# Performance work log

Hardware: AMD Instinct MI355X
Metric: run time of the kernel (lower is better)

The kernel has to match this reference:

```python
import jax, jax.numpy as jnp
import numpy as np
import math

B, N0 = 128, 128          # graphs, nodes per graph
EPG = 512                 # edges per graph
F_IN, EDGE_DIM = 64, 16
EMB, HEADS = 128, 4
HC = EMB * HEADS
L = 2                     # stacked layers (pooling every layer: top_k_every_n=1)
RATIO = 0.5
DENSE = 256


def setup_inputs():
    rng = np.random.default_rng(0)

    def U(fan_in, *shape):
        s = 1.0 / np.sqrt(fan_in)
        return jnp.asarray(rng.uniform(-s, s, shape), dtype=jnp.float32)

    x = jnp.asarray(rng.standard_normal((B * N0, F_IN)), dtype=jnp.float32)
    src = rng.integers(0, N0, (B, EPG))
    dst = rng.integers(0, N0, (B, EPG))
    off = (np.arange(B) * N0)[:, None]
    edge_index = jnp.asarray(np.stack([(src + off).reshape(-1), (dst + off).reshape(-1)]), dtype=jnp.int32)
    edge_attr = jnp.asarray(rng.standard_normal((B * EPG, EDGE_DIM)), dtype=jnp.float32)

    inp = dict(x=x, edge_index=edge_index, edge_attr=edge_attr)
    inp.update(
        c1_Wq=U(F_IN, F_IN, HC), c1_bq=U(F_IN, HC),
        c1_Wk=U(F_IN, F_IN, HC), c1_bk=U(F_IN, HC),
        c1_Wv=U(F_IN, F_IN, HC), c1_bv=U(F_IN, HC),
        c1_We=U(EDGE_DIM, EDGE_DIM, HC),
        c1_Ws=U(F_IN, F_IN, HC), c1_bs=U(F_IN, HC),
        c1_Wb=U(3 * HC, 3 * HC),
        t1_W=U(HC, HC, EMB), t1_b=U(HC, EMB),
        bn1_g=jnp.ones(EMB), bn1_b=jnp.zeros(EMB),
        cl_Wq=U(EMB, L, EMB, HC), cl_bq=U(EMB, L, HC),
        cl_Wk=U(EMB, L, EMB, HC), cl_bk=U(EMB, L, HC),
        cl_Wv=U(EMB, L, EMB, HC), cl_bv=U(EMB, L, HC),
        cl_We=U(EDGE_DIM, L, EDGE_DIM, HC),
        cl_Ws=U(EMB, L, EMB, HC), cl_bs=U(EMB, L, HC),
        cl_Wb=U(3 * HC, L, 3 * HC),
        tl_W=U(HC, L, HC, EMB), tl_b=U(HC, L, EMB),
        bnl_g=jnp.ones((L, EMB)), bnl_b=jnp.zeros((L, EMB)),
        pool_w=U(EMB, L, EMB),
        l1_W=U(2 * EMB, 2 * EMB, DENSE), l1_b=U(2 * EMB, DENSE),
        l2_W=U(DENSE, DENSE, DENSE // 2), l2_b=U(DENSE, DENSE // 2),
        l3_W=U(DENSE // 2, DENSE // 2, 1), l3_b=U(DENSE // 2, 1),
    )
    return inp


def _tconv(x, src, dst, emask, ea, Wq, bq, Wk, bk, Wv, bv, We, Ws, bs, Wb, n_nodes):
    # PyG TransformerConv, beta=True, concat=True, edge features added to key and value
    H, C = HEADS, EMB
    q = (x @ Wq + bq).reshape(-1, H, C)
    k = (x @ Wk + bk).reshape(-1, H, C)
    v = (x @ Wv + bv).reshape(-1, H, C)
    e = (ea @ We).reshape(-1, H, C)
    kj = k[src] + e
    alpha = (q[dst] * kj).sum(-1) * (1.0 / math.sqrt(C))  # [E, H]
    mx = jax.ops.segment_max(jnp.where(emask[:, None], alpha, -jnp.inf), dst, num_segments=n_nodes)
    mx = jnp.where(jnp.isfinite(mx), mx, 0.0)
    p = jnp.where(emask[:, None], jnp.exp(alpha - mx[dst]), 0.0)
    p = p / (jax.ops.segment_sum(p, dst, num_segments=n_nodes)[dst] + 1e-16)
    msg = v[src] + e
    out = jax.ops.segment_sum(p[:, :, None] * msg, dst, num_segments=n_nodes).reshape(-1, H * C)
    skip = x @ Ws + bs
    beta = jax.nn.sigmoid(jnp.concatenate([out, skip, out - skip], -1) @ Wb)[:, None]
    return beta * skip + (1.0 - beta) * out


def _bn(x, g, b):
    # BatchNorm1d, training-mode batch statistics (biased variance)
    m = x.mean(0)
    v = ((x - m) ** 2).mean(0)
    return g * (x - m) * jax.lax.rsqrt(v + 1e-5) + b


def _topk_pool(x, src, dst, emask, w, n):
    # TopKPooling: score = x.w/|w|, keep top ceil(ratio*n) per graph, scale by tanh(score)
    k = int(math.ceil(RATIO * n))
    s = (x @ w) / jnp.linalg.norm(w)          # [B*n]
    _, idx = jax.lax.top_k(s.reshape(B, n), k)
    idx = jnp.sort(idx, axis=1)
    gidx = (jnp.arange(B)[:, None] * n + idx).reshape(-1)
    x_new = x[gidx] * jnp.tanh(s[gidx])[:, None]
    kept = jnp.zeros(B * n, bool).at[gidx].set(True)
    new_id = (jnp.cumsum(kept) - 1).astype(jnp.int32)
    em = emask & kept[src] & kept[dst]
    src_n = jnp.where(em, new_id[src], 0)
    dst_n = jnp.where(em, new_id[dst], 0)
    return x_new, src_n, dst_n, em, k


def _forward(edge_index, x, edge_attr, c1_Wq, c1_bq, c1_Wk, c1_bk, c1_Wv, c1_bv, c1_We, c1_Ws, c1_bs, c1_Wb,
             t1_W, t1_b, bn1_g, bn1_b, cl_Wq, cl_bq, cl_Wk, cl_bk, cl_Wv, cl_bv, cl_We, cl_Ws, cl_bs, cl_Wb,
             tl_W, tl_b, bnl_g, bnl_b, pool_w, l1_W, l1_b, l2_W, l2_b, l3_W, l3_b):
    src, dst = edge_index[0], edge_index[1]
    emask = jnp.ones(src.shape[0], bool)
    n = N0
    x = _tconv(x, src, dst, emask, edge_attr, c1_Wq, c1_bq, c1_Wk, c1_bk, c1_Wv, c1_bv, c1_We, c1_Ws, c1_bs, c1_Wb, B * n)
    x = _bn(jax.nn.relu(x @ t1_W + t1_b), bn1_g, bn1_b)
    reps = []
    for i in range(L):
        x = _tconv(x, src, dst, emask, edge_attr, cl_Wq[i], cl_bq[i], cl_Wk[i], cl_bk[i], cl_Wv[i], cl_bv[i],
                   cl_We[i], cl_Ws[i], cl_bs[i], cl_Wb[i], B * n)
        x = _bn(jax.nn.relu(x @ tl_W[i] + tl_b[i]), bnl_g[i], bnl_b[i])
        x, src, dst, emask, n = _topk_pool(x, src, dst, emask, pool_w[i], n)
        xg = x.reshape(B, n, EMB)
        reps.append(jnp.concatenate([xg.max(1), xg.mean(1)], -1))  # gmp || gap
    h = reps[0]
    for r in reps[1:]:
        h = h + r
    h = jax.nn.relu(h @ l1_W + l1_b)  # dropout p=0.8 is identity at eval
    h = jax.nn.relu(h @ l2_W + l2_b)
    return h @ l3_W + l3_b            # [B, 1]


def reference(x, edge_index, edge_attr, c1_Wq, c1_bq, c1_Wk, c1_bk, c1_Wv, c1_bv, c1_We, c1_Ws, c1_bs, c1_Wb,
              t1_W, t1_b, bn1_g, bn1_b, cl_Wq, cl_bq, cl_Wk, cl_bk, cl_Wv, cl_bv, cl_We, cl_Ws, cl_bs, cl_Wb,
              tl_W, tl_b, bnl_g, bnl_b, pool_w, l1_W, l1_b, l2_W, l2_b, l3_W, l3_b):
    return _forward(edge_index, x, edge_attr, c1_Wq, c1_bq, c1_Wk, c1_bk, c1_Wv, c1_bv, c1_We, c1_Ws, c1_bs, c1_Wb,
                    t1_W, t1_b, bn1_g, bn1_b, cl_Wq, cl_bq, cl_Wk, cl_bk, cl_Wv, cl_bv, cl_We, cl_Ws, cl_bs, cl_Wb,
                    tl_W, tl_b, bnl_g, bnl_b, pool_w, l1_W, l1_b, l2_W, l2_b, l3_W, l3_b)
```

## Files before the change

kernel.cpp:

```cpp
#include <hip/hip_runtime.h>
#include <math.h>

#define E_TOT 65536
#define B_G   128
#define QLD   1664
#define NCOL  1792

typedef __attribute__((ext_vector_type(8))) short short8;
typedef __attribute__((ext_vector_type(4))) short short4v;
typedef __attribute__((ext_vector_type(4))) float float4v;

__device__ __forceinline__ unsigned short f2bf(float f) {
    unsigned int u = __float_as_uint(f);
    unsigned int r = u + 0x7FFFu + ((u >> 16) & 1u);
    return (unsigned short)(r >> 16);
}
__device__ __forceinline__ float bf2f(unsigned short h) {
    return __uint_as_float(((unsigned int)h) << 16);
}

struct LayerPrep {
    const float *Ws, *bs_, *Wq, *bq, *We, *Wv, *bv, *tW;
    float *Wst, *ws_z, *sbt, *zb, *Wu, *bu, *Wet, *wez, *Wvt, *bvt, *Wvz, *bvz, *tWT;
    unsigned short *Whi, *Wlo;
    int Fin;
};

__device__ __forceinline__ LayerPrep pick(const LayerPrep& p0, const LayerPrep& p1,
                                          const LayerPrep& p2) {
    return blockIdx.y == 0 ? p0 : (blockIdx.y == 1 ? p1 : p2);
}

__global__ void twt_all_k(LayerPrep p0, LayerPrep p1, LayerPrep p2) {
    LayerPrep p = pick(p0, p1, p2);
    int idx = blockIdx.x * 256 + threadIdx.x;
    int m = idx & 127, c = idx >> 7;
    p.tWT[m * 512 + c] = p.tW[idx];
}

__global__ void prep_all_k(LayerPrep p0, LayerPrep p1, LayerPrep p2, const float* Wb0,
                           const float* Wb1, const float* Wb2) {
    LayerPrep p = pick(p0, p1, p2);
    const float* Wb = blockIdx.y == 0 ? Wb0 : (blockIdx.y == 1 ? Wb1 : Wb2);
    int Fin = p.Fin;
    int w = (blockIdx.x * blockDim.x + threadIdx.x) >> 6;
    int lane = threadIdx.x & 63;
    int o1 = Fin * 128, o2 = o1 + Fin, o3 = o2 + 128, o4 = o3 + 1;
    int o5 = o4 + Fin * 64, o6 = o5 + 64, o7 = o6 + 8192, o8 = o7 + 64;
    int o9 = o8 + Fin * 512, o10 = o9 + 512, o11 = o10 + Fin * 4, total = o11 + 4;
    if (w >= total) return;
    const float *Ws = p.Ws, *bs = p.bs_, *tWT = p.tWT, *Wq = p.Wq, *bq = p.bq,
                *We = p.We, *Wv = p.Wv, *bv = p.bv;
    float s = 0.f;
    if (w < o1) {
        int f = w >> 7, m = w & 127;
        for (int c = lane; c < 512; c += 64)
            s = fmaf(Ws[(size_t)f * 512 + c], tWT[(size_t)m * 512 + c], s);
    } else if (w < o2) {
        int f = w - o1;
        for (int c = lane; c < 512; c += 64)
            s = fmaf(Ws[(size_t)f * 512 + c], Wb[512 + c] - Wb[1024 + c], s);
    } else if (w < o3) {
        int m = w - o2;
        for (int c = lane; c < 512; c += 64)
            s = fmaf(bs[c], tWT[(size_t)m * 512 + c], s);
    } else if (w < o4) {
        for (int c = lane; c < 512; c += 64)
            s = fmaf(bs[c], Wb[512 + c] - Wb[1024 + c], s);
    } else if (w < o5) {
        int q = w - o4; int f = q >> 6; int j2 = q & 63;
        int j = j2 & 15; int cb = (j2 >> 4) * 128;
        s = Wq[(size_t)f * 512 + cb + lane] * We[j * 512 + cb + lane]
          + Wq[(size_t)f * 512 + cb + lane + 64] * We[j * 512 + cb + lane + 64];
    } else if (w < o6) {
        int j2 = w - o5; int j = j2 & 15; int cb = (j2 >> 4) * 128;
        s = bq[cb + lane] * We[j * 512 + cb + lane]
          + bq[cb + lane + 64] * We[j * 512 + cb + lane + 64];
    } else if (w < o7) {
        int q = w - o6; int j2 = q >> 7; int m = q & 127;
        int j = j2 & 15; int cb = (j2 >> 4) * 128;
        s = We[j * 512 + cb + lane] * tWT[(size_t)m * 512 + cb + lane]
          + We[j * 512 + cb + lane + 64] * tWT[(size_t)m * 512 + cb + lane + 64];
    } else if (w < o8) {
        int j2 = w - o7; int j = j2 & 15; int cb = (j2 >> 4) * 128;
        s = We[j * 512 + cb + lane] * (Wb[cb + lane] + Wb[1024 + cb + lane])
          + We[j * 512 + cb + lane + 64] * (Wb[cb + lane + 64] + Wb[1024 + cb + lane + 64]);
    } else if (w < o9) {
        int q = w - o8; int f = q >> 9; int j2 = q & 511;
        int cb = (j2 >> 7) * 128; int m = j2 & 127;
        s = Wv[(size_t)f * 512 + cb + lane] * tWT[(size_t)m * 512 + cb + lane]
          + Wv[(size_t)f * 512 + cb + lane + 64] * tWT[(size_t)m * 512 + cb + lane + 64];
    } else if (w < o10) {
        int j2 = w - o9; int cb = (j2 >> 7) * 128; int m = j2 & 127;
        s = bv[cb + lane] * tWT[(size_t)m * 512 + cb + lane]
          + bv[cb + lane + 64] * tWT[(size_t)m * 512 + cb + lane + 64];
    } else if (w < o11) {
        int q = w - o10; int f = q >> 2; int cb = (q & 3) * 128;
        s = Wv[(size_t)f * 512 + cb + lane] * (Wb[cb + lane] + Wb[1024 + cb + lane])
          + Wv[(size_t)f * 512 + cb + lane + 64] * (Wb[cb + lane + 64] + Wb[1024 + cb + lane + 64]);
    } else {
        int cb = (w - o11) * 128;
        s = bv[cb + lane] * (Wb[cb + lane] + Wb[1024 + cb + lane])
          + bv[cb + lane + 64] * (Wb[cb + lane + 64] + Wb[1024 + cb + lane + 64]);
    }
#pragma unroll
    for (int off = 32; off; off >>= 1) s += __shfl_xor(s, off, 64);
    if (lane == 0) {
        if (w < o1) p.Wst[w] = s;
        else if (w < o2) p.ws_z[w - o1] = s;
        else if (w < o3) p.sbt[w - o2] = s;
        else if (w < o4) p.zb[0] = s;
        else if (w < o5) p.Wu[w - o4] = s;
        else if (w < o6) p.bu[w - o5] = s;
        else if (w < o7) p.Wet[w - o6] = s;
        else if (w < o8) p.wez[w - o7] = s;
        else if (w < o9) p.Wvt[w - o8] = s;
        else if (w < o10) p.bvt[w - o9] = s;
        else if (w < o11) p.Wvz[w - o10] = s;
        else p.bvz[w - o11] = s;
    }
}

__global__ void wsplit_all_k(LayerPrep p0, LayerPrep p1, LayerPrep p2,
                             const float* Wk0, const float* Wk1, const float* Wk2) {
    LayerPrep p = pick(p0, p1, p2);
    const float* Wk = blockIdx.y == 0 ? Wk0 : (blockIdx.y == 1 ? Wk1 : Wk2);
    int K = p.Fin, kshift = (K == 64) ? 6 : 7;
    int idx = blockIdx.x * 256 + threadIdx.x;
    if (idx >= NCOL * K) return;
    int col = idx >> kshift, k = idx & (K - 1);
    float w;
    if (col < 128)       w = p.Wst[k * 128 + col];
    else if (col < 640)  w = p.Wq[(size_t)k * 512 + col - 128];
    else if (col < 1152) w = Wk[(size_t)k * 512 + col - 640];
    else if (col < 1664) w = p.Wvt[(size_t)k * 512 + col - 1152];
    else if (col < 1728) w = p.Wu[(size_t)k * 64 + col - 1664];
    else if (col < 1732) w = p.Wvz[(size_t)k * 4 + col - 1728];
    else if (col == 1732) w = p.ws_z[k];
    else                 w = 0.f;
    unsigned short h = f2bf(w);
    p.Whi[idx] = h;
    p.Wlo[idx] = f2bf(w - bf2f(h));
}

__global__ void xsplit_k(const float* __restrict__ X, int total4,
                         unsigned short* __restrict__ Xhi, unsigned short* __restrict__ Xlo) {
    int idx = blockIdx.x * 256 + threadIdx.x;
    if (idx >= total4) return;
    float4 f = ((const float4*)X)[idx];
    unsigned short h0 = f2bf(f.x), h1 = f2bf(f.y), h2 = f2bf(f.z), h3 = f2bf(f.w);
    short4v hv = {(short)h0, (short)h1, (short)h2, (short)h3};
    short4v lv = {(short)f2bf(f.x - bf2f(h0)), (short)f2bf(f.y - bf2f(h1)),
                  (short)f2bf(f.z - bf2f(h2)), (short)f2bf(f.w - bf2f(h3))};
    *(short4v*)(Xhi + (size_t)idx * 4) = hv;
    *(short4v*)(Xlo + (size_t)idx * 4) = lv;
}

template <int KT>
__global__ __launch_bounds__(256) void qkvs_mfma(
        const unsigned short* __restrict__ Xhi, const unsigned short* __restrict__ Xlo,
        const unsigned short* __restrict__ Whi, const unsigned short* __restrict__ Wlo,
        const float* __restrict__ bq, const float* __restrict__ bk,
        const float* __restrict__ bvt, const float* __restrict__ bu,
        const float* __restrict__ bvz, const float* __restrict__ zb,
        float* __restrict__ out, float* __restrict__ UB, float* __restrict__ VZB,
        float* __restrict__ SZB, int nwg8) {
    constexpr int NKC = KT >> 5;
    constexpr int NCH = KT >> 6;
    __shared__ __align__(16) unsigned short bs[NCH * 2 * 64 * 80];
    const int ldb = 80;
    int tid = threadIdx.x;
    int wave = tid >> 6, lane = tid & 63;
    int m = lane & 15, kg = lane >> 4;
    int hw = blockIdx.y * 28 + blockIdx.x;
    int lb = (hw & 7) * nwg8 + (hw >> 3);
    int rb = (lb / 28) * 256;
    int c0 = (lb % 28) * 64;

    short8 ahi[2][NKC], alo[2][NKC];
    auto loadA = [&](int n0) {
#pragma unroll
        for (int rt = 0; rt < 2; ++rt) {
            const unsigned short* xh = Xhi + (size_t)(n0 + rt * 16 + m) * KT + kg * 8;
            const unsigned short* xl = Xlo + (size_t)(n0 + rt * 16 + m) * KT + kg * 8;
#pragma unroll
            for (int kc = 0; kc < NKC; ++kc) {
                ahi[rt][kc] = *(const short8*)(xh + kc * 32);
                alo[rt][kc] = *(const short8*)(xl + kc * 32);
            }
        }
    };
    loadA(rb + wave * 32);

    for (int i = tid; i < NCH * 64 * 8; i += 256) {
        int ch = i >> 9;
        int r = i & 511; int col = r >> 3, part = r & 7;
        unsigned short* dst = bs + ch * (2 * 64 * 80);
        *(short8*)(dst + col * ldb + part * 8) =
            *(const short8*)(Whi + (size_t)(c0 + col) * KT + ch * 64 + part * 8);
        *(short8*)(dst + 64 * 80 + col * ldb + part * 8) =
            *(const short8*)(Wlo + (size_t)(c0 + col) * KT + ch * 64 + part * 8);
    }
    __syncthreads();

    float bias[4];
#pragma unroll
    for (int ct = 0; ct < 4; ++ct) {
        int col = c0 + ct * 16 + m;
        float bv_;
        if (col < 128)       bv_ = 0.f;
        else if (col < 640)  bv_ = bq[col - 128];
        else if (col < 1152) bv_ = bk[col - 640];
        else if (col < 1664) bv_ = bvt[col - 1152];
        else if (col < 1728) bv_ = bu[col - 1664];
        else if (col < 1732) bv_ = bvz[col - 1728];
        else if (col == 1732) bv_ = zb[0];
        else                 bv_ = 0.f;
        bias[ct] = bv_;
    }

#pragma unroll
    for (int rg = 0; rg < 2; ++rg) {
        int n0 = rb + rg * 128 + wave * 32;
        if (rg) loadA(n0);

        float4v acc[2][4];
#pragma unroll
        for (int rt = 0; rt < 2; ++rt)
#pragma unroll
            for (int ct = 0; ct < 4; ++ct) acc[rt][ct] = (float4v){0.f, 0.f, 0.f, 0.f};

#pragma unroll
        for (int ch = 0; ch < NCH; ++ch) {
            const unsigned short* bsc = bs + ch * (2 * 64 * 80);
#pragma unroll
            for (int kc2 = 0; kc2 < 2; ++kc2) {
                const int kc = ch * 2 + kc2;
#pragma unroll
                for (int ct = 0; ct < 4; ++ct) {
                    const unsigned short* bp = bsc + (ct * 16 + m) * ldb + kg * 8 + kc2 * 32;
                    short8 bhi = *(const short8*)(bp);
                    short8 blo = *(const short8*)(bp + 64 * 80);
                    acc[0][ct] = __builtin_amdgcn_mfma_f32_16x16x32_bf16(ahi[0][kc], bhi, acc[0][ct], 0, 0, 0);
                    acc[0][ct] = __builtin_amdgcn_mfma_f32_16x16x32_bf16(alo[0][kc], bhi, acc[0][ct], 0, 0, 0);
                    acc[0][ct] = __builtin_amdgcn_mfma_f32_16x16x32_bf16(ahi[0][kc], blo, acc[0][ct], 0, 0, 0);
                    acc[1][ct] = __builtin_amdgcn_mfma_f32_16x16x32_bf16(ahi[1][kc], bhi, acc[1][ct], 0, 0, 0);
                    acc[1][ct] = __builtin_amdgcn_mfma_f32_16x16x32_bf16(alo[1][kc], bhi, acc[1][ct], 0, 0, 0);
                    acc[1][ct] = __builtin_amdgcn_mfma_f32_16x16x32_bf16(ahi[1][kc], blo, acc[1][ct], 0, 0, 0);
                }
            }
        }

#pragma unroll
        for (int ct = 0; ct < 4; ++ct) {
            int col = c0 + ct * 16 + m;
            if (col > 1732) continue;
#pragma unroll
            for (int rt = 0; rt < 2; ++rt) {
#pragma unroll
                for (int r = 0; r < 4; ++r) {
                    int row = n0 + rt * 16 + kg * 4 + r;
                    float v = acc[rt][ct][r] + bias[ct];
                    if (col < 1664)      out[(size_t)row * QLD + col] = v;
                    else if (col < 1728) UB[(size_t)row * 64 + col - 1664] = v;
                    else if (col < 1732) VZB[(size_t)row * 4 + col - 1728] = v;
                    else                 SZB[row] = v;
                }
            }
        }
    }
}

__global__ __launch_bounds__(128) void csr_graph_k(const int* __restrict__ src,
                                                   const int* __restrict__ dst,
                                                   int* __restrict__ row_start,
                                                   int* __restrict__ row_end,
                                                   int* __restrict__ colb,
                                                   int* __restrict__ eidb) {
    __shared__ int cnt[128], pref[128], cur[128];
    int g = blockIdx.x, t = threadIdx.x;
    cnt[t] = 0;
    __syncthreads();
    int e0 = g * 512, nb = g * 128;
    int dl[4], sl[4];
#pragma unroll
    for (int i = 0; i < 4; ++i) {
        int e = e0 + t + i * 128;
        dl[i] = dst[e] - nb;
        sl[i] = src[e];
        atomicAdd(&cnt[dl[i]], 1);
    }
    __syncthreads();
    pref[t] = cnt[t];
    __syncthreads();
    for (int st = 1; st < 128; st <<= 1) {
        int v = (t >= st) ? pref[t - st] : 0;
        __syncthreads();
        pref[t] += v;
        __syncthreads();
    }
    int ex = pref[t] - cnt[t];
    row_start[nb + t] = e0 + ex;
    row_end[nb + t]   = e0 + pref[t];
    cur[t] = ex;
    __syncthreads();
#pragma unroll
    for (int i = 0; i < 4; ++i) {
        int pos = atomicAdd(&cur[dl[i]], 1);
        colb[e0 + pos] = sl[i];
        eidb[e0 + pos] = e0 + t + i * 128;
    }
}

__global__ __launch_bounds__(256) void attn_combine_k(
        const float* __restrict__ QB, const float* __restrict__ UB,
        const float* __restrict__ VZB, const float* __restrict__ SZB,
        const int* __restrict__ row_start, const int* __restrict__ row_end,
        const int* __restrict__ colb, const int* __restrict__ eidb,
        const float* __restrict__ ea, const float* __restrict__ wez,
        const float* __restrict__ Wet, const float* __restrict__ sbt,
        const float* __restrict__ tb, float* __restrict__ xn, int nwg8) {
    __shared__ float shO[4][4][128];
    __shared__ float tsh[4][64];
    __shared__ float zsh[4][4];
    int tid = threadIdx.x;
    int head = tid >> 6, lane = tid & 63;
    int grp = lane >> 4, li = lane & 15;
    int bid = blockIdx.x;
    int lb = (bid & 7) * nwg8 + (bid >> 3);
    int node = lb * 4 + grp;

    float wezv = wez[head * 16 + li];
    const float* Qr = QB + (size_t)node * QLD + 128 + head * 128 + li * 8;
    float4 q0 = *(const float4*)Qr;
    float4 q1 = *(const float4*)(Qr + 4);
    float uu = UB[(size_t)node * 64 + head * 16 + li];
    int beg = row_start[node], end = row_end[node];

    float l = 0.f, t = 0.f, zac = 0.f;
    float4 a0 = {0.f, 0.f, 0.f, 0.f}, a1 = {0.f, 0.f, 0.f, 0.f};
    const float scale = 0.08838834764831845f;
    int j = beg;
    for (; j + 1 < end; j += 2) {
        int s1 = colb[j],     e1 = eidb[j];
        int s2 = colb[j + 1], e2 = eidb[j + 1];
        const float* K1 = QB + (size_t)s1 * QLD + 640 + head * 128 + li * 8;
        const float* V1 = QB + (size_t)s1 * QLD + 1152 + head * 128 + li * 8;
        const float* K2 = QB + (size_t)s2 * QLD + 640 + head * 128 + li * 8;
        const float* V2 = QB + (size_t)s2 * QLD + 1152 + head * 128 + li * 8;
        float4 k10 = *(const float4*)K1, k11 = *(const float4*)(K1 + 4);
        float4 v10 = *(const float4*)V1, v11 = *(const float4*)(V1 + 4);
        float4 k20 = *(const float4*)K2, k21 = *(const float4*)(K2 + 4);
        float4 v20 = *(const float4*)V2, v21 = *(const float4*)(V2 + 4);
        float ea1 = ea[(size_t)e1 * 16 + li];
        float ea2 = ea[(size_t)e2 * 16 + li];
        float vz1 = VZB[(size_t)s1 * 4 + head];
        float vz2 = VZB[(size_t)s2 * 4 + head];
        float p1 = q0.x * k10.x + q0.y * k10.y + q0.z * k10.z + q0.w * k10.w
                 + q1.x * k11.x + q1.y * k11.y + q1.z * k11.z + q1.w * k11.w + ea1 * uu;
        float p2 = q0.x * k20.x + q0.y * k20.y + q0.z * k20.z + q0.w * k20.w
                 + q1.x * k21.x + q1.y * k21.y + q1.z * k21.z + q1.w * k21.w + ea2 * uu;
        p1 += __shfl_xor(p1, 1, 64); p1 += __shfl_xor(p1, 2, 64);
        p1 += __shfl_xor(p1, 4, 64); p1 += __shfl_xor(p1, 8, 64);
        p2 += __shfl_xor(p2, 1, 64); p2 += __shfl_xor(p2, 2, 64);
        p2 += __shfl_xor(p2, 4, 64); p2 += __shfl_xor(p2, 8, 64);
        float w1 = expf(p1 * scale), w2 = expf(p2 * scale);
        l += w1; l += w2;
        t = fmaf(w1, ea1, t); t = fmaf(w2, ea2, t);
        zac = fmaf(w1, vz1, zac); zac = fmaf(w2, vz2, zac);
        a0.x = fmaf(w1, v10.x, a0.x); a0.y = fmaf(w1, v10.y, a0.y);
        a0.z = fmaf(w1, v10.z, a0.z); a0.w = fmaf(w1, v10.w, a0.w);
        a1.x = fmaf(w1, v11.x, a1.x); a1.y = fmaf(w1, v11.y, a1.y);
        a1.z = fmaf(w1, v11.z, a1.z); a1.w = fmaf(w1, v11.w, a1.w);
        a0.x = fmaf(w2, v20.x, a0.x); a0.y = fmaf(w2, v20.y, a0.y);
        a0.z = fmaf(w2, v20.z, a0.z); a0.w = fmaf(w2, v20.w, a0.w);
        a1.x = fmaf(w2, v21.x, a1.x); a1.y = fmaf(w2, v21.y, a1.y);
        a1.z = fmaf(w2, v21.z, a1.z); a1.w = fmaf(w2, v21.w, a1.w);
    }
    if (j < end) {
        int s1 = colb[j], e1 = eidb[j];
        const float* K1 = QB + (size_t)s1 * QLD + 640 + head * 128 + li * 8;
        const float* V1 = QB + (size_t)s1 * QLD + 1152 + head * 128 + li * 8;
        float4 k10 = *(const float4*)K1, k11 = *(const float4*)(K1 + 4);
        float4 v10 = *(const float4*)V1, v11 = *(const float4*)(V1 + 4);
        float ea1 = ea[(size_t)e1 * 16 + li];
        float vz1 = VZB[(size_t)s1 * 4 + head];
        float p1 = q0.x * k10.x + q0.y * k10.y + q0.z * k10.z + q0.w * k10.w
                 + q1.x * k11.x + q1.y * k11.y + q1.z * k11.z + q1.w * k11.w + ea1 * uu;
        p1 += __shfl_xor(p1, 1, 64); p1 += __shfl_xor(p1, 2, 64);
        p1 += __shfl_xor(p1, 4, 64); p1 += __shfl_xor(p1, 8, 64);
        float w1 = expf(p1 * scale);
        l += w1;
        t = fmaf(w1, ea1, t);
        zac = fmaf(w1, vz1, zac);
        a0.x = fmaf(w1, v10.x, a0.x); a0.y = fmaf(w1, v10.y, a0.y);
        a0.z = fmaf(w1, v10.z, a0.z); a0.w = fmaf(w1, v10.w, a0.w);
        a1.x = fmaf(w1, v11.x, a1.x); a1.y = fmaf(w1, v11.y, a1.y);
        a1.z = fmaf(w1, v11.z, a1.z); a1.w = fmaf(w1, v11.w, a1.w);
    }

    float inv = 1.f / (l + 1e-16f);
    float tn = t * inv;
    float zw = tn * wezv;
    zw += __shfl_xor(zw, 1, 64); zw += __shfl_xor(zw, 2, 64);
    zw += __shfl_xor(zw, 4, 64); zw += __shfl_xor(zw, 8, 64);
    float z = zac * inv + zw;

    float* op = &shO[grp][head][li * 8];
    op[0] = a0.x * inv; op[1] = a0.y * inv; op[2] = a0.z * inv; op[3] = a0.w * inv;
    op[4] = a1.x * inv; op[5] = a1.y * inv; op[6] = a1.z * inv; op[7] = a1.w * inv;
    tsh[grp][head * 16 + li] = tn;
    if (li == 0) zsh[grp][head] = z;
    __syncthreads();

    int dim = tid & 127;
    int nsBase = tid >> 7;
    float sb = sbt[dim], tbv = tb[dim];
    float wet0 = 0.f, wet1 = 0.f;
#pragma unroll 8
    for (int jj = 0; jj < 64; ++jj) {
        float wv = Wet[jj * 128 + dim];
        wet0 = fmaf(tsh[nsBase][jj], wv, wet0);
        wet1 = fmaf(tsh[nsBase + 2][jj], wv, wet1);
    }
#pragma unroll
    for (int r = 0; r < 2; ++r) {
        int ns = nsBase + r * 2;
        float wet = r ? wet1 : wet0;
        int nd = lb * 4 + ns;
        float outT = shO[ns][0][dim] + shO[ns][1][dim] + shO[ns][2][dim] + shO[ns][3][dim] + wet;
        float zt = zsh[ns][0] + zsh[ns][1] + zsh[ns][2] + zsh[ns][3] + SZB[nd];
        float beta = 1.f / (1.f + expf(-zt));
        float S = QB[(size_t)nd * QLD + dim];
        float a = beta * (S + sb) + (1.f - beta) * outT + tbv;
        xn[(size_t)nd * 128 + dim] = fmaxf(a, 0.f);
    }
}

__global__ void bn_stats_k(const float* __restrict__ x, int N, float* __restrict__ stats) {
    int c = threadIdx.x;
    float s = 0.f, ss = 0.f;
    for (int n = blockIdx.x; n < N; n += gridDim.x) {
        float v = x[(size_t)n * 128 + c];
        s += v; ss += v * v;
    }
    atomicAdd(&stats[c], s);
    atomicAdd(&stats[128 + c], ss);
}

__global__ void bn_apply_k(float* __restrict__ x, int N, const float* __restrict__ stats,
                           const float* __restrict__ g, const float* __restrict__ b,
                           unsigned short* __restrict__ Xhi, unsigned short* __restrict__ Xlo) {
    int idx = blockIdx.x * blockDim.x + threadIdx.x;
    if (idx >= N * 128) return;
    int c = idx & 127;
    float m = stats[c] / (float)N;
    float var = fmaxf(stats[128 + c] / (float)N - m * m, 0.f);
    float inv = rsqrtf(var + 1e-5f);
    float v = g[c] * (x[idx] - m) * inv + b[c];
    x[idx] = v;
    unsigned short h = f2bf(v);
    Xhi[idx] = h;
    Xlo[idx] = f2bf(v - bf2f(h));
}

__global__ void bn_apply_score_k(float* __restrict__ x, int N, const float* __restrict__ stats,
                                 const float* __restrict__ g, const float* __restrict__ b,
                                 const float* __restrict__ w, float* __restrict__ s) {
    int node = blockIdx.x * 4 + (threadIdx.x >> 6);
    int lane = threadIdx.x & 63;
    int c0 = lane, c1 = lane + 64;
    float m0 = stats[c0] / (float)N;
    float v0 = fmaxf(stats[128 + c0] / (float)N - m0 * m0, 0.f);
    float m1 = stats[c1] / (float)N;
    float v1 = fmaxf(stats[128 + c1] / (float)N - m1 * m1, 0.f);
    float* row = x + (size_t)node * 128;
    float x0 = g[c0] * (row[c0] - m0) * rsqrtf(v0 + 1e-5f) + b[c0];
    float x1 = g[c1] * (row[c1] - m1) * rsqrtf(v1 + 1e-5f) + b[c1];
    row[c0] = x0;
    row[c1] = x1;
    float w0 = w[c0], w1 = w[c1];
    float p  = x0 * w0 + x1 * w1;
    float nw = w0 * w0 + w1 * w1;
#pragma unroll
    for (int off = 32; off; off >>= 1) {
        p  += __shfl_xor(p, off, 64);
        nw += __shfl_xor(nw, off, 64);
    }
    if (lane == 0) s[node] = p / sqrtf(nw);
}

__global__ __launch_bounds__(128) void topk_pool0_k(
        const float* __restrict__ sc, const float* __restrict__ x,
        const int* __restrict__ src, const int* __restrict__ dst,
        float* __restrict__ xp, float* __restrict__ rep,
        int* __restrict__ row_start, int* __restrict__ row_end,
        int* __restrict__ colb, int* __restrict__ eidb,
        unsigned short* __restrict__ Xhi, unsigned short* __restrict__ Xlo) {
    __shared__ float ls[128], th[64];
    __shared__ int lk[128], rk[128], oon[64];
    __shared__ int cnt[64], pref[64], cur[64];
    int g = blockIdx.x, t = threadIdx.x;
    float val = sc[g * 128 + t];
    ls[t] = val;
    __syncthreads();
    int c = 0;
    for (int j = 0; j < 128; ++j) {
        float vj = ls[j];
        c += (vj > val || (vj == val && j < t)) ? 1 : 0;
    }
    int kp = (c < 64) ? 1 : 0;
    lk[t] = kp;
    __syncthreads();
    int r = 0;
    for (int j = 0; j < t; ++j) r += lk[j];
    rk[t] = r;
    if (kp) { oon[r] = t; th[r] = tanhf(val); }
    __syncthreads();
    float mx = -INFINITY, sm = 0.f;
    for (int rr = 0; rr < 64; ++rr) {
        float v = x[(size_t)(g * 128 + oon[rr]) * 128 + t] * th[rr];
        int oidx = (g * 64 + rr) * 128 + t;
        xp[oidx] = v;
        unsigned short h = f2bf(v);
        Xhi[oidx] = h;
        Xlo[oidx] = f2bf(v - bf2f(h));
        mx = fmaxf(mx, v);
        sm += v;
    }
    rep[g * 256 + t] = mx;
    rep[g * 256 + 128 + t] = sm * (1.f / 64.f);
    if (t < 64) cnt[t] = 0;
    __syncthreads();
    int e0 = g * 512, nb = g * 128;
    int keepE[4], dr[4], sr[4];
#pragma unroll
    for (int i = 0; i < 4; ++i) {
        int e = e0 + t + i * 128;
        int s_ = src[e] - nb, d_ = dst[e] - nb;
        int ke = lk[s_] && lk[d_];
        keepE[i] = ke;
        dr[i] = rk[d_];
        sr[i] = rk[s_];
        if (ke) atomicAdd(&cnt[dr[i]], 1);
    }
    __syncthreads();
    if (t < 64) pref[t] = cnt[t];
    __syncthreads();
    for (int st = 1; st < 64; st <<= 1) {
        int v = (t < 64 && t >= st) ? pref[t - st] : 0;
        __syncthreads();
        if (t < 64) pref[t] += v;
        __syncthreads();
    }
    if (t < 64) {
        int ex = pref[t] - cnt[t];
        row_start[g * 64 + t] = e0 + ex;
        row_end[g * 64 + t]   = e0 + pref[t];
        cur[t] = ex;
    }
    __syncthreads();
#pragma unroll
    for (int i = 0; i < 4; ++i) {
        if (keepE[i]) {
            int pos = atomicAdd(&cur[dr[i]], 1);
            colb[e0 + pos] = g * 64 + sr[i];
            eidb[e0 + pos] = e0 + t + i * 128;
        }
    }
}

__global__ __launch_bounds__(128) void topk_pool1_k(
        const float* __restrict__ sc, const float* __restrict__ x,
        float* __restrict__ rep) {
    __shared__ float ls[64], th[32];
    __shared__ int lk[64], oon[32];
    int g = blockIdx.x, t = threadIdx.x;
    float val = 0.f;
    if (t < 64) { val = sc[g * 64 + t]; ls[t] = val; }
    __syncthreads();
    if (t < 64) {
        int c = 0;
        for (int j = 0; j < 64; ++j) {
            float vj = ls[j];
            c += (vj > val || (vj == val && j < t)) ? 1 : 0;
        }
        int kp = (c < 32) ? 1 : 0;
        lk[t] = kp;
    }
    __syncthreads();
    if (t < 64 && lk[t]) {
        int r = 0;
        for (int j = 0; j < t; ++j) r += lk[j];
        oon[r] = t;
        th[r] = tanhf(val);
    }
    __syncthreads();
    float mx = -INFINITY, sm = 0.f;
    for (int rr = 0; rr < 32; ++rr) {
        float v = x[(size_t)(g * 64 + oon[rr]) * 128 + t] * th[rr];
        mx = fmaxf(mx, v);
        sm += v;
    }
    rep[g * 256 + t] = mx;
    rep[g * 256 + 128 + t] = sm * (1.f / 32.f);
}

__global__ void head_k(const float* __restrict__ rep0, const float* __restrict__ rep1,
                       const float* __restrict__ W1, const float* __restrict__ b1,
                       const float* __restrict__ W2, const float* __restrict__ b2,
                       const float* __restrict__ W3, const float* __restrict__ b3,
                       float* __restrict__ out) {
    __shared__ float h[256], a1[256], a2[128], red[256];
    int g = blockIdx.x, t = threadIdx.x;
    h[t] = rep0[g * 256 + t] + rep1[g * 256 + t];
    __syncthreads();
    float acc = b1[t];
    for (int i = 0; i < 256; ++i) acc = fmaf(h[i], W1[i * 256 + t], acc);
    a1[t] = fmaxf(acc, 0.f);
    __syncthreads();
    if (t < 128) {
        float a = b2[t];
        for (int i = 0; i < 256; ++i) a = fmaf(a1[i], W2[i * 128 + t], a);
        a2[t] = fmaxf(a, 0.f);
    }
    __syncthreads();
    red[t] = (t < 128) ? a2[t] * W3[t] : 0.f;
    __syncthreads();
    for (int st = 128; st; st >>= 1) {
        if (t < st) red[t] += red[t + st];
        __syncthreads();
    }
    if (t == 0) out[g] = red[0] + b3[0];
}

extern "C" void kernel_launch(void* const* d_in, const int* in_sizes, int n_in,
                              void* d_out, int out_size, void* d_ws, size_t ws_size,
                              hipStream_t stream) {
    (void)in_sizes; (void)n_in; (void)out_size; (void)ws_size;

    const float* x0    = (const float*)d_in[0];
    const int*   ei    = (const int*)d_in[1];
    const float* ea    = (const float*)d_in[2];
    const float* c1_Wq = (const float*)d_in[3];
    const float* c1_bq = (const float*)d_in[4];
    const float* c1_Wk = (const float*)d_in[5];
    const float* c1_bk = (const float*)d_in[6];
    const float* c1_Wv = (const float*)d_in[7];
    const float* c1_bv = (const float*)d_in[8];
    const float* c1_We = (const float*)d_in[9];
    const float* c1_Ws = (const float*)d_in[10];
    const float* c1_bs = (const float*)d_in[11];
    const float* c1_Wb = (const float*)d_in[12];
    const float* t1_W  = (const float*)d_in[13];
    const float* t1_b  = (const float*)d_in[14];
    const float* bn1_g = (const float*)d_in[15];
    const float* bn1_b = (const float*)d_in[16];
    const float* cl_Wq = (const float*)d_in[17];
    const float* cl_bq = (const float*)d_in[18];
    const float* cl_Wk = (const float*)d_in[19];
    const float* cl_bk = (const float*)d_in[20];
    const float* cl_Wv = (const float*)d_in[21];
    const float* cl_bv = (const float*)d_in[22];
    const float* cl_We = (const float*)d_in[23];
    const float* cl_Ws = (const float*)d_in[24];
    const float* cl_bs = (const float*)d_in[25];
    const float* cl_Wb = (const float*)d_in[26];
    const float* tl_W  = (const float*)d_in[27];
    const float* tl_b  = (const float*)d_in[28];
    const float* bnl_g = (const float*)d_in[29];
    const float* bnl_b = (const float*)d_in[30];
    const float* pool_w= (const float*)d_in[31];
    const float* l1_W  = (const float*)d_in[32];
    const float* l1_b  = (const float*)d_in[33];
    const float* l2_W  = (const float*)d_in[34];
    const float* l2_b  = (const float*)d_in[35];
    const float* l3_W  = (const float*)d_in[36];
    const float* l3_b  = (const float*)d_in[37];
    float* out = (float*)d_out;

    char* base = (char*)d_ws;
    size_t off = 0;
    auto alloc = [&](size_t bytes) -> void* {
        void* p = base + off;
        off += (bytes + 255) & ~(size_t)255;
        return p;
    };
    float* QB   = (float*)alloc((size_t)16384 * QLD * 4);
    float* xA   = (float*)alloc((size_t)16384 * 128 * 4);
    float* xB   = (float*)alloc((size_t)16384 * 128 * 4);
    float* UB   = (float*)alloc((size_t)16384 * 64 * 4);
    float* VZB  = (float*)alloc((size_t)16384 * 4 * 4);
    float* SZB  = (float*)alloc((size_t)16384 * 4);
    float* stats  = (float*)alloc(256 * 4);
    float* scores = (float*)alloc(16384 * 4);
    float* rep0   = (float*)alloc(128 * 256 * 4);
    float* rep1   = (float*)alloc(128 * 256 * 4);
    int* row_start = (int*)alloc(16384 * 4);
    int* row_end   = (int*)alloc(16384 * 4);
    int* colb      = (int*)alloc(E_TOT * 4);
    int* eidb      = (int*)alloc(E_TOT * 4);
    unsigned short* Xhi = (unsigned short*)alloc((size_t)16384 * 128 * 2);
    unsigned short* Xlo = (unsigned short*)alloc((size_t)16384 * 128 * 2);

    LayerPrep P[3];
    const float* Wb_[3] = {c1_Wb, cl_Wb, cl_Wb + 1536};
    const float* Wk_[3] = {c1_Wk, cl_Wk, cl_Wk + 65536};
    for (int l = 0; l < 3; ++l) {
        LayerPrep& p = P[l];
        p.Wst  = (float*)alloc(128 * 128 * 4);
        p.ws_z = (float*)alloc(128 * 4);
        p.sbt  = (float*)alloc(128 * 4);
        p.zb   = (float*)alloc(16);
        p.Wu   = (float*)alloc(128 * 64 * 4);
        p.bu   = (float*)alloc(64 * 4);
        p.Wet  = (float*)alloc(64 * 128 * 4);
        p.wez  = (float*)alloc(64 * 4);
        p.Wvt  = (float*)alloc(128 * 512 * 4);
        p.bvt  = (float*)alloc(512 * 4);
        p.Wvz  = (float*)alloc(128 * 4 * 4);
        p.bvz  = (float*)alloc(16);
        p.tWT  = (float*)alloc(128 * 512 * 4);
        p.Whi  = (unsigned short*)alloc((size_t)NCOL * 128 * 2);
        p.Wlo  = (unsigned short*)alloc((size_t)NCOL * 128 * 2);
    }
    P[0].Ws = c1_Ws; P[0].bs_ = c1_bs; P[0].Wq = c1_Wq; P[0].bq = c1_bq;
    P[0].We = c1_We; P[0].Wv = c1_Wv; P[0].bv = c1_bv; P[0].tW = t1_W; P[0].Fin = 64;
    P[1].Ws = cl_Ws; P[1].bs_ = cl_bs; P[1].Wq = cl_Wq; P[1].bq = cl_bq;
    P[1].We = cl_We; P[1].Wv = cl_Wv; P[1].bv = cl_bv; P[1].tW = tl_W; P[1].Fin = 128;
    P[2].Ws = cl_Ws + 65536; P[2].bs_ = cl_bs + 512; P[2].Wq = cl_Wq + 65536;
    P[2].bq = cl_bq + 512; P[2].We = cl_We + 8192; P[2].Wv = cl_Wv + 65536;
    P[2].bv = cl_bv + 512; P[2].tW = tl_W + 65536; P[2].Fin = 128;

    float* xp = xA;

    twt_all_k<<<dim3(256, 3), 256, 0, stream>>>(P[0], P[1], P[2]);
    {
        int totalMax = 128 * 128 + 128 + 129 + 128 * 64 + 64 + 8192 + 64
                     + 128 * 512 + 512 + 128 * 4 + 4;
        prep_all_k<<<dim3((totalMax + 3) / 4, 3), 256, 0, stream>>>(P[0], P[1], P[2],
                                                                    Wb_[0], Wb_[1], Wb_[2]);
        wsplit_all_k<<<dim3((NCOL * 128 + 255) / 256, 3), 256, 0, stream>>>(P[0], P[1], P[2],
                                                                            Wk_[0], Wk_[1], Wk_[2]);
    }

    csr_graph_k<<<B_G, 128, 0, stream>>>(ei, ei + E_TOT, row_start, row_end, colb, eidb);
    xsplit_k<<<(16384 * 64 / 4 + 255) / 256, 256, 0, stream>>>(x0, 16384 * 64 / 4, Xhi, Xlo);

    auto tconv = [&](int L, int N, const float* bq, const float* bk, const float* tb,
                     float* xn) {
        int nwg8 = 28 * (N / 256) / 8;
        if (P[L].Fin == 64)
            qkvs_mfma<64><<<dim3(28, N / 256), 256, 0, stream>>>(Xhi, Xlo, P[L].Whi, P[L].Wlo,
                                                                 bq, bk, P[L].bvt, P[L].bu,
                                                                 P[L].bvz, P[L].zb,
                                                                 QB, UB, VZB, SZB, nwg8);
        else
            qkvs_mfma<128><<<dim3(28, N / 256), 256, 0, stream>>>(Xhi, Xlo, P[L].Whi, P[L].Wlo,
                                                                  bq, bk, P[L].bvt, P[L].bu,
                                                                  P[L].bvz, P[L].zb,
                                                                  QB, UB, VZB, SZB, nwg8);
        attn_combine_k<<<N / 4, 256, 0, stream>>>(QB, UB, VZB, SZB,
                                                  row_start, row_end, colb, eidb,
                                                  ea, P[L].wez, P[L].Wet, P[L].sbt, tb,
                                                  xn, N / 32);
    };

    tconv(0, 16384, c1_bq, c1_bk, t1_b, xA);
    hipMemsetAsync(stats, 0, 256 * 4, stream);
    bn_stats_k<<<512, 128, 0, stream>>>(xA, 16384, stats);
    bn_apply_k<<<(16384 * 128 + 255) / 256, 256, 0, stream>>>(xA, 16384, stats, bn1_g, bn1_b,
                                                              Xhi, Xlo);

    tconv(1, 16384, cl_bq, cl_bk, tl_b, xB);
    hipMemsetAsync(stats, 0, 256 * 4, stream);
    bn_stats_k<<<512, 128, 0, stream>>>(xB, 16384, stats);
    bn_apply_score_k<<<16384 / 4, 256, 0, stream>>>(xB, 16384, stats, bnl_g, bnl_b,
                                                    pool_w, scores);

    topk_pool0_k<<<B_G, 128, 0, stream>>>(scores, xB, ei, ei + E_TOT, xp, rep0,
                                          row_start, row_end, colb, eidb, Xhi, Xlo);

    tconv(2, 8192, cl_bq + 512, cl_bk + 512, tl_b + 128, xB);
    hipMemsetAsync(stats, 0, 256 * 4, stream);
    bn_stats_k<<<512, 128, 0, stream>>>(xB, 8192, stats);
    bn_apply_score_k<<<8192 / 4, 256, 0, stream>>>(xB, 8192, stats, bnl_g + 128, bnl_b + 128,
                                                   pool_w + 128, scores);

    topk_pool1_k<<<B_G, 128, 0, stream>>>(scores, xB, rep1);

    head_k<<<B_G, 256, 0, stream>>>(rep0, rep1, l1_W, l1_b, l2_W, l2_b, l3_W, l3_b, out);
}
```

Baseline: 570.8 us.

## Fuse weight-fold prep matvecs to read tW directly, drop transpose kernel

Removes the separate transpose kernel that built tWT and restructures the weight-folding prep so each wavefront computes 64 output columns at once, reading rows of tW with coalesced lane-contiguous loads. This replaces one-wave-per-output-scalar dot products with shuffle reductions by per-lane sequential accumulation over four partial sums. The prep grid shrinks substantially. It cuts launch count and reduction overhead in weight preprocessing, at the cost of longer serial loops per lane.

```diff
diff --git a/kernel.cpp b/kernel.cpp
--- a/kernel.cpp
+++ b/kernel.cpp
@@ -21,7 +21,7 @@
 
 struct LayerPrep {
     const float *Ws, *bs_, *Wq, *bq, *We, *Wv, *bv, *tW;
-    float *Wst, *ws_z, *sbt, *zb, *Wu, *bu, *Wet, *wez, *Wvt, *bvt, *Wvz, *bvz, *tWT;
+    float *Wst, *ws_z, *sbt, *zb, *Wu, *bu, *Wet, *wez, *Wvt, *bvt, *Wvz, *bvz;
     unsigned short *Whi, *Wlo;
     int Fin;
 };
@@ -29,13 +29,6 @@
 __device__ __forceinline__ LayerPrep pick(const LayerPrep& p0, const LayerPrep& p1,
                                           const LayerPrep& p2) {
     return blockIdx.y == 0 ? p0 : (blockIdx.y == 1 ? p1 : p2);
-}
-
-__global__ void twt_all_k(LayerPrep p0, LayerPrep p1, LayerPrep p2) {
-    LayerPrep p = pick(p0, p1, p2);
-    int idx = blockIdx.x * 256 + threadIdx.x;
-    int m = idx & 127, c = idx >> 7;
-    p.tWT[m * 512 + c] = p.tW[idx];
 }
 
 __global__ void prep_all_k(LayerPrep p0, LayerPrep p1, LayerPrep p2, const float* Wb0,
@@ -43,81 +36,95 @@
     LayerPrep p = pick(p0, p1, p2);
     const float* Wb = blockIdx.y == 0 ? Wb0 : (blockIdx.y == 1 ? Wb1 : Wb2);
     int Fin = p.Fin;
-    int w = (blockIdx.x * blockDim.x + threadIdx.x) >> 6;
+    int w = blockIdx.x * 4 + (threadIdx.x >> 6);
     int lane = threadIdx.x & 63;
-    int o1 = Fin * 128, o2 = o1 + Fin, o3 = o2 + 128, o4 = o3 + 1;
-    int o5 = o4 + Fin * 64, o6 = o5 + 64, o7 = o6 + 8192, o8 = o7 + 64;
-    int o9 = o8 + Fin * 512, o10 = o9 + 512, o11 = o10 + Fin * 4, total = o11 + 4;
-    if (w >= total) return;
-    const float *Ws = p.Ws, *bs = p.bs_, *tWT = p.tWT, *Wq = p.Wq, *bq = p.bq,
-                *We = p.We, *Wv = p.Wv, *bv = p.bv;
+
+    int U1 = Fin * 2;
+    int U2 = U1 + 2;
+    int U3 = U2 + Fin * 8;
+    int U4 = U3 + 8;
+    int U5 = U4 + 128;
+    if (w < U5) {
+        const float* A; const float* bp; float* outp; int R;
+        if (w < U1) {
+            int f = w >> 1, m0 = (w & 1) * 64;
+            A = p.Ws + (size_t)f * 512; bp = p.tW + m0 + lane;
+            outp = p.Wst + f * 128 + m0 + lane; R = 512;
+        } else if (w < U2) {
+            int m0 = (w - U1) * 64;
+            A = p.bs_; bp = p.tW + m0 + lane;
+            outp = p.sbt + m0 + lane; R = 512;
+        } else if (w < U3) {
+            int u = w - U2; int f = u >> 3, q = u & 7;
+            int cb = (q >> 1) * 128, m0 = (q & 1) * 64;
+            A = p.Wv + (size_t)f * 512 + cb; bp = p.tW + cb * 128 + m0 + lane;
+            outp = p.Wvt + (size_t)f * 512 + q * 64 + lane; R = 128;
+        } else if (w < U4) {
+            int q = w - U3; int cb = (q >> 1) * 128, m0 = (q & 1) * 64;
+            A = p.bv + cb; bp = p.tW + cb * 128 + m0 + lane;
+            outp = p.bvt + q * 64 + lane; R = 128;
+        } else {
+            int u = w - U4; int j2 = u >> 1, m0 = (u & 1) * 64;
+            int j = j2 & 15, cb = (j2 >> 4) * 128;
+            A = p.We + j * 512 + cb; bp = p.tW + cb * 128 + m0 + lane;
+            outp = p.Wet + j2 * 128 + m0 + lane; R = 128;
+        }
+        float a0 = 0.f, a1 = 0.f, a2 = 0.f, a3 = 0.f;
+        for (int c = 0; c < R; c += 4) {
+            a0 = fmaf(A[c],     bp[0],   a0);
+            a1 = fmaf(A[c + 1], bp[128], a1);
+            a2 = fmaf(A[c + 2], bp[256], a2);
+            a3 = fmaf(A[c + 3], bp[384], a3);
+            bp += 512;
+        }
+        *outp = (a0 + a1) + (a2 + a3);
+        return;
+    }
+
+    int w2 = w - U5;
+    int q1 = Fin, q2 = q1 + 1, q3 = q2 + Fin * 64, q4 = q3 + 64, q5 = q4 + 64;
+    int q6 = q5 + Fin * 4, q7 = q6 + 4;
+    if (w2 >= q7) return;
     float s = 0.f;
-    if (w < o1) {
-        int f = w >> 7, m = w & 127;
+    if (w2 < q1) {
+        int f = w2;
         for (int c = lane; c < 512; c += 64)
-            s = fmaf(Ws[(size_t)f * 512 + c], tWT[(size_t)m * 512 + c], s);
-    } else if (w < o2) {
-        int f = w - o1;
+            s = fmaf(p.Ws[(size_t)f * 512 + c], Wb[512 + c] - Wb[1024 + c], s);
+    } else if (w2 < q2) {
         for (int c = lane; c < 512; c += 64)
-            s = fmaf(Ws[(size_t)f * 512 + c], Wb[512 + c] - Wb[1024 + c], s);
-    } else if (w < o3) {
-        int m = w - o2;
-        for (int c = lane; c < 512; c += 64)
-            s = fmaf(bs[c], tWT[(size_t)m * 512 + c], s);
-    } else if (w < o4) {
-        for (int c = lane; c < 512; c += 64)
-            s = fmaf(bs[c], Wb[512 + c] - Wb[1024 + c], s);
-    } else if (w < o5) {
-        int q = w - o4; int f = q >> 6; int j2 = q & 63;
+            s = fmaf(p.bs_[c], Wb[512 + c] - Wb[1024 + c], s);
+    } else if (w2 < q3) {
+        int q = w2 - q2; int f = q >> 6; int j2 = q & 63;
         int j = j2 & 15; int cb = (j2 >> 4) * 128;
-        s = Wq[(size_t)f * 512 + cb + lane] * We[j * 512 + cb + lane]
-          + Wq[(size_t)f * 512 + cb + lane + 64] * We[j * 512 + cb + lane + 64];
-    } else if (w < o6) {
-        int j2 = w - o5; int j = j2 & 15; int cb = (j2 >> 4) * 128;
-        s = bq[cb + lane] * We[j * 512 + cb + lane]
-          + bq[cb + lane + 64] * We[j * 512 + cb + lane + 64];
-    } else if (w < o7) {
-        int q = w - o6; int j2 = q >> 7; int m = q & 127;
-        int j = j2 & 15; int cb = (j2 >> 4) * 128;
-        s = We[j * 512 + cb + lane] * tWT[(size_t)m * 512 + cb + lane]
-          + We[j * 512 + cb + lane + 64] * tWT[(size_t)m * 512 + cb + lane + 64];
-    } else if (w < o8) {
-        int j2 = w - o7; int j = j2 & 15; int cb = (j2 >> 4) * 128;
-        s = We[j * 512 + cb + lane] * (Wb[cb + lane] + Wb[1024 + cb + lane])
-          + We[j * 512 + cb + lane + 64] * (Wb[cb + lane + 64] + Wb[1024 + cb + lane + 64]);
-    } else if (w < o9) {
-        int q = w - o8; int f = q >> 9; int j2 = q & 511;
-        int cb = (j2 >> 7) * 128; int m = j2 & 127;
-        s = Wv[(size_t)f * 512 + cb + lane] * tWT[(size_t)m * 512 + cb + lane]
-          + Wv[(size_t)f * 512 + cb + lane + 64] * tWT[(size_t)m * 512 + cb + lane + 64];
-    } else if (w < o10) {
-        int j2 = w - o9; int cb = (j2 >> 7) * 128; int m = j2 & 127;
-        s = bv[cb + lane] * tWT[(size_t)m * 512 + cb + lane]
-          + bv[cb + lane + 64] * tWT[(size_t)m * 512 + cb + lane + 64];
-    } else if (w < o11) {
-        int q = w - o10; int f = q >> 2; int cb = (q & 3) * 128;
-        s = Wv[(size_t)f * 512 + cb + lane] * (Wb[cb + lane] + Wb[1024 + cb + lane])
-          + Wv[(size_t)f * 512 + cb + lane + 64] * (Wb[cb + lane + 64] + Wb[1024 + cb + lane + 64]);
+        s = p.Wq[(size_t)f * 512 + cb + lane] * p.We[j * 512 + cb + lane]
+          + p.Wq[(size_t)f * 512 + cb + lane + 64] * p.We[j * 512 + cb + lane + 64];
+    } else if (w2 < q4) {
+        int j2 = w2 - q3; int j = j2 & 15; int cb = (j2 >> 4) * 128;
+        s = p.bq[cb + lane] * p.We[j * 512 + cb + lane]
+          + p.bq[cb + lane + 64] * p.We[j * 512 + cb + lane + 64];
+    } else if (w2 < q5) {
+        int j2 = w2 - q4; int j = j2 & 15; int cb = (j2 >> 4) * 128;
+        s = p.We[j * 512 + cb + lane] * (Wb[cb + lane] + Wb[1024 + cb + lane])
+          + p.We[j * 512 + cb + lane + 64] * (Wb[cb + lane + 64] + Wb[1024 + cb + lane + 64]);
+    } else if (w2 < q6) {
+        int q = w2 - q5; int f = q >> 2; int cb = (q & 3) * 128;
+        s = p.Wv[(size_t)f * 512 + cb + lane] * (Wb[cb + lane] + Wb[1024 + cb + lane])
+          + p.Wv[(size_t)f * 512 + cb + lane + 64] * (Wb[cb + lane + 64] + Wb[1024 + cb + lane + 64]);
     } else {
-        int cb = (w - o11) * 128;
-        s = bv[cb + lane] * (Wb[cb + lane] + Wb[1024 + cb + lane])
-          + bv[cb + lane + 64] * (Wb[cb + lane + 64] + Wb[1024 + cb + lane + 64]);
+        int cb = (w2 - q6) * 128;
+        s = p.bv[cb + lane] * (Wb[cb + lane] + Wb[1024 + cb + lane])
+          + p.bv[cb + lane + 64] * (Wb[cb + lane + 64] + Wb[1024 + cb + lane + 64]);
     }
 #pragma unroll
     for (int off = 32; off; off >>= 1) s += __shfl_xor(s, off, 64);
     if (lane == 0) {
-        if (w < o1) p.Wst[w] = s;
-        else if (w < o2) p.ws_z[w - o1] = s;
-        else if (w < o3) p.sbt[w - o2] = s;
-        else if (w < o4) p.zb[0] = s;
-        else if (w < o5) p.Wu[w - o4] = s;
-        else if (w < o6) p.bu[w - o5] = s;
-        else if (w < o7) p.Wet[w - o6] = s;
-        else if (w < o8) p.wez[w - o7] = s;
-        else if (w < o9) p.Wvt[w - o8] = s;
-        else if (w < o10) p.bvt[w - o9] = s;
-        else if (w < o11) p.Wvz[w - o10] = s;
-        else p.bvz[w - o11] = s;
+        if (w2 < q1) p.ws_z[w2] = s;
+        else if (w2 < q2) p.zb[0] = s;
+        else if (w2 < q3) p.Wu[w2 - q2] = s;
+        else if (w2 < q4) p.bu[w2 - q3] = s;
+        else if (w2 < q5) p.wez[w2 - q4] = s;
+        else if (w2 < q6) p.Wvz[w2 - q5] = s;
+        else p.bvz[w2 - q6] = s;
     }
 }
 
@@ -720,7 +727,6 @@
         p.bvt  = (float*)alloc(512 * 4);
         p.Wvz  = (float*)alloc(128 * 4 * 4);
         p.bvz  = (float*)alloc(16);
-        p.tWT  = (float*)alloc(128 * 512 * 4);
         p.Whi  = (unsigned short*)alloc((size_t)NCOL * 128 * 2);
         p.Wlo  = (unsigned short*)alloc((size_t)NCOL * 128 * 2);
     }
@@ -734,11 +740,9 @@
 
     float* xp = xA;
 
-    twt_all_k<<<dim3(256, 3), 256, 0, stream>>>(P[0], P[1], P[2]);
     {
-        int totalMax = 128 * 128 + 128 + 129 + 128 * 64 + 64 + 8192 + 64
-                     + 128 * 512 + 512 + 128 * 4 + 4;
-        prep_all_k<<<dim3((totalMax + 3) / 4, 3), 256, 0, stream>>>(P[0], P[1], P[2],
+        int unitsMax = (10 * 128 + 138) + (69 * 128 + 133);
+        prep_all_k<<<dim3((unitsMax + 3) / 4, 3), 256, 0, stream>>>(P[0], P[1], P[2],
                                                                     Wb_[0], Wb_[1], Wb_[2]);
         wsplit_all_k<<<dim3((NCOL * 128 + 255) / 256, 3), 256, 0, stream>>>(P[0], P[1], P[2],
                                                                             Wk_[0], Wk_[1], Wk_[2]);
```

Result: faster. 521.8 us (-8.6%).
